# Performance work log

Measured on AMD Instinct MI355X. Metric: run time of the kernel, lower is better.

Reference implementation:

```python
import jax, jax.numpy as jnp
import numpy as np

N = 50000
E = 640000
F_IN = 128
HID = 128
OUT = 64


def setup_inputs() -> dict:
    key = jax.random.key(0)
    ks = jax.random.split(key, 16)
    x = jax.random.normal(ks[0], (N, F_IN), dtype=jnp.float32)
    edge_index = jax.random.randint(ks[1], (2, E), 0, N, dtype=jnp.int64)

    def lin(k, fan_in, fan_out):
        bound = 1.0 / np.sqrt(fan_in)
        kw, kb = jax.random.split(k)
        W = jax.random.uniform(kw, (fan_in, fan_out), jnp.float32, -bound, bound)
        b = jax.random.uniform(kb, (fan_out,), jnp.float32, -bound, bound)
        return W, b

    W1, b1 = lin(ks[2], F_IN, HID)
    W2, b2 = lin(ks[3], HID, HID)
    W3, b3 = lin(ks[4], HID, HID)
    Wres, bres = lin(ks[5], F_IN, HID)
    Wlin, blin = lin(ks[6], HID, OUT)
    return {"x": x, "edge_index": edge_index,
            "W1": W1, "b1": b1, "W2": W2, "b2": b2, "W3": W3, "b3": b3,
            "Wres": Wres, "bres": bres, "Wlin": Wlin, "blin": blin}


def _gcn_norm(edge_index, n):
    # GCNConv default: add self-loops, symmetric normalization D^-1/2 (A+I) D^-1/2
    src, dst = edge_index[0], edge_index[1]
    deg = jax.ops.segment_sum(jnp.ones((edge_index.shape[1],), jnp.float32), dst,
                              num_segments=n) + 1.0  # +1 for self-loop
    dinv = jax.lax.rsqrt(deg)
    norm_e = dinv[src] * dinv[dst]          # [E] edge coefficients
    norm_self = 1.0 / deg                    # [N] self-loop coefficients
    return src, dst, norm_e, norm_self


def _gcn_conv(x, W, b, src, dst, norm_e, norm_self, n):
    h = x @ W                                # [N, F_out]
    agg = jax.ops.segment_sum(h[src] * norm_e[:, None], dst, num_segments=n)
    agg = agg + h * norm_self[:, None]       # self-loop contribution
    return agg + b


def reference(x, edge_index, W1, b1, W2, b2, W3, b3, Wres, bres, Wlin, blin):
    n = x.shape[0]
    src, dst, norm_e, norm_self = _gcn_norm(edge_index, n)
    x_res = x @ Wres + bres
    h = _gcn_conv(x, W1, b1, src, dst, norm_e, norm_self, n)
    h = jax.nn.relu(h + x_res)               # dropout is identity in eval mode
    h = _gcn_conv(h, W2, b2, src, dst, norm_e, norm_self, n)
    h = jax.nn.relu(h)
    h = _gcn_conv(h, W3, b3, src, dst, norm_e, norm_self, n)
    h = jax.nn.relu(h)
    return h @ Wlin + blin
```

## Files before the change

kernel.cpp:

```cpp
#include <hip/hip_runtime.h>

typedef unsigned short ushort_t;
typedef unsigned int uint_t;

typedef __bf16 bf16x8 __attribute__((ext_vector_type(8)));
typedef float f32x4 __attribute__((ext_vector_type(4)));

union BFU { ushort_t u; __bf16 h; };

__device__ __forceinline__ float bf2f(uint_t u) {
    union { uint_t i; float f; } v; v.i = u << 16; return v.f;
}
__device__ __forceinline__ ushort_t f2bf(float f) {
    union { float f; uint_t i; } v; v.f = f;
    uint_t r = v.i + 0x7fffu + ((v.i >> 16) & 1u);
    return (ushort_t)(r >> 16);
}
__device__ __forceinline__ float loadF(const void* p, size_t i, int isBf16) {
    return isBf16 ? bf2f((uint_t)((const ushort_t*)p)[i]) : ((const float*)p)[i];
}

struct DetectArgs {
    const void* t[11];
    int elems[11];
    const int* ei;
    int* flags;
};

__device__ __forceinline__ int detect_one(const void* p, int elems) {
    const uint_t* w = (const uint_t*)p;
    int n = elems / 2; if (n > 64) n = 64;
    int cnt = 0;
    for (int k = 0; k < n; ++k) {
        uint_t f = (w[k] >> 7) & 0xFFu;
        cnt += (f >= 100u && f <= 135u);
    }
    return (cnt * 10 >= n * 6) ? 1 : 0;
}

__global__ void k_pack(DetectArgs a,
                       ushort_t* __restrict__ Tcat, ushort_t* __restrict__ T2,
                       ushort_t* __restrict__ T3, ushort_t* __restrict__ Tl,
                       int* __restrict__ deg, int N,
                       ushort_t* __restrict__ Hbuf, int hps) {
    __shared__ int lflag;
    int i = blockIdx.x * blockDim.x + threadIdx.x;
    if (i < N) deg[i] = 0;
    if (blockIdx.x == 1 && threadIdx.x < 64) {
        int p = threadIdx.x >> 4, w = threadIdx.x & 15;
        ((uint_t*)Hbuf)[(size_t)p * (hps / 2) + (size_t)N * 16 + w] = 0u;
    }
    const int SQ = 128 * 128;
    int m = (i < 4 * SQ) ? (i / SQ) : 4;
    int fid = (m == 0) ? 1 : (m == 1) ? 3 : (m == 2) ? 5 : (m == 3) ? 7 : 9;
    const void* W = a.t[fid];

    if (threadIdx.x == 0) lflag = detect_one(W, a.elems[fid]);
    if (blockIdx.x == 0 && threadIdx.x >= 64 && threadIdx.x < 75) {
        int t = threadIdx.x - 64;
        a.flags[t] = detect_one(a.t[t], a.elems[t]);
    }
    if (blockIdx.x == 0 && threadIdx.x == 75) {
        int nz = 0;
        for (int k = 0; k < 64; ++k) nz += (a.ei[2 * k + 1] != 0);
        a.flags[11] = (nz == 0) ? 1 : 0;
    }
    __syncthreads();
    int isb = lflag;

    if (i < 4 * SQ) {
        int r = i % SQ;
        int k = r / 128, f = r % 128;
        ushort_t* T = (m == 0) ? Tcat : (m == 1) ? T2 : (m == 2) ? T3 : (Tcat + SQ);
        T[f * 128 + k] = f2bf(loadF(W, (size_t)k * 128 + f, isb));
    } else if (i < 4 * SQ + 128 * 64) {
        int r = i - 4 * SQ;
        int k = r / 64, f = r % 64;
        Tl[f * 128 + k] = f2bf(loadF(W, (size_t)k * 64 + f, isb));
    }
}

__global__ void k_deg(const int* __restrict__ ei, int E, int N,
                      const int* __restrict__ flags, int* __restrict__ deg,
                      int2* __restrict__ tmp) {
    int i = blockIdx.x * blockDim.x + threadIdx.x;
    int e0 = i * 4;
    if (e0 >= E) return;
    int is64 = flags[11];
    if (e0 + 3 < E && (E & 3) == 0) {
        int d[4];
        if (is64) {
            int4 va = *(const int4*)(ei + 2 * E + 2 * e0);
            int4 vb = *(const int4*)(ei + 2 * E + 2 * e0 + 4);
            d[0] = va.x; d[1] = va.z; d[2] = vb.x; d[3] = vb.z;
        } else {
            int4 va = *(const int4*)(ei + E + e0);
            d[0] = va.x; d[1] = va.y; d[2] = va.z; d[3] = va.w;
        }
        int l[4]; bool ok[4];
#pragma unroll
        for (int k = 0; k < 4; ++k) ok[k] = (unsigned)d[k] < (unsigned)N;
#pragma unroll
        for (int k = 0; k < 4; ++k)
            l[k] = ok[k] ? atomicAdd(&deg[d[k]], 1) : 0;
        int4 t01, t23;
        t01.x = ok[0] ? d[0] : -1; t01.y = l[0];
        t01.z = ok[1] ? d[1] : -1; t01.w = l[1];
        t23.x = ok[2] ? d[2] : -1; t23.y = l[2];
        t23.z = ok[3] ? d[3] : -1; t23.w = l[3];
        *(int4*)(tmp + e0) = t01;
        *(int4*)(tmp + e0 + 2) = t23;
    } else {
        for (int e = e0; e < E && e < e0 + 4; ++e) {
            int dd = is64 ? ei[2 * E + 2 * e] : ei[E + e];
            bool ok = (unsigned)dd < (unsigned)N;
            int l = ok ? atomicAdd(&deg[dd], 1) : 0;
            tmp[e] = make_int2(ok ? dd : -1, l);
        }
    }
}


__global__ __launch_bounds__(256) void k_bsum(const int* __restrict__ deg, int n,
                                              int* __restrict__ bsum) {
    int base = blockIdx.x * 1024;
    int local = 0;
#pragma unroll
    for (int j = 0; j < 4; ++j) {
        int idx = base + threadIdx.x + j * 256;
        if (idx < n) local += deg[idx];
    }
    __shared__ int s[4];
#pragma unroll
    for (int off = 32; off; off >>= 1) local += __shfl_down(local, off, 64);
    if ((threadIdx.x & 63) == 0) s[threadIdx.x >> 6] = local;
    __syncthreads();
    if (threadIdx.x == 0) bsum[blockIdx.x] = s[0] + s[1] + s[2] + s[3];
}

__global__ __launch_bounds__(256) void k_rowptr(const int* __restrict__ deg,
                                                const int* __restrict__ bsum, int n,
                                                int* __restrict__ row_ptr,
                                                float* __restrict__ dinv) {
    __shared__ int s[256];
    __shared__ int sboff;
    int t = threadIdx.x;

    if (t < 64) {
        int v = (t < blockIdx.x) ? bsum[t] : 0;
#pragma unroll
        for (int off = 32; off; off >>= 1) v += __shfl_down(v, off, 64);
        if (t == 0) sboff = v;
    }

    int base = blockIdx.x * 1024 + t * 4;
    int v0 = (base + 0 < n) ? deg[base + 0] : 0;
    int v1 = (base + 1 < n) ? deg[base + 1] : 0;
    int v2 = (base + 2 < n) ? deg[base + 2] : 0;
    int v3 = (base + 3 < n) ? deg[base + 3] : 0;
    int tot = v0 + v1 + v2 + v3;
    s[t] = tot;
    __syncthreads();
    for (int off = 1; off < 256; off <<= 1) {
        int u = (t >= off) ? s[t - off] : 0;
        __syncthreads();
        s[t] += u;
        __syncthreads();
    }
    int run = sboff + ((t == 0) ? 0 : s[t - 1]);
    int vals[4] = {v0, v1, v2, v3};
#pragma unroll
    for (int j = 0; j < 4; ++j) {
        int idx = base + j;
        if (idx < n) {
            row_ptr[idx] = run;
            run += vals[j];
            float df = (float)vals[j] + 1.0f;
            dinv[idx] = rsqrtf(df);
        }
    }
    if (blockIdx.x == gridDim.x - 1 && t == 255) row_ptr[n] = sboff + s[255];
}

__global__ void k_scatter(const int* __restrict__ ei, int E, int N,
                          const int* __restrict__ flags,
                          const int* __restrict__ row_ptr,
                          const int2* __restrict__ tmp,
                          uint_t* __restrict__ colw) {
    int i = blockIdx.x * blockDim.x + threadIdx.x;
    int e0 = i * 4;
    if (e0 >= E) return;
    int is64 = flags[11];
    if (e0 + 3 < E && (E & 3) == 0) {
        int s[4];
        if (is64) {
            int4 sa = *(const int4*)(ei + 2 * e0);
            int4 sb = *(const int4*)(ei + 2 * e0 + 4);
            s[0] = sa.x; s[1] = sa.z; s[2] = sb.x; s[3] = sb.z;
        } else {
            int4 sa = *(const int4*)(ei + e0);
            s[0] = sa.x; s[1] = sa.y; s[2] = sa.z; s[3] = sa.w;
        }
        int4 t01 = *(const int4*)(tmp + e0);
        int4 t23 = *(const int4*)(tmp + e0 + 2);
        int d[4] = {t01.x, t01.z, t23.x, t23.z};
        int l[4] = {t01.y, t01.w, t23.y, t23.w};
        int ss[4];
#pragma unroll
        for (int k = 0; k < 4; ++k)
            ss[k] = ((unsigned)s[k] < (unsigned)N) ? s[k] : 0;
#pragma unroll
        for (int k = 0; k < 4; ++k) {
            if (d[k] >= 0)
                colw[row_ptr[d[k]] + l[k]] = (uint_t)ss[k];
        }
    } else {
        for (int e = e0; e < E && e < e0 + 4; ++e) {
            int sv = is64 ? ei[2 * e] : ei[e];
            int2 tv = tmp[e];
            if (tv.x >= 0) {
                int ssv = ((unsigned)sv < (unsigned)N) ? sv : 0;
                colw[row_ptr[tv.x] + tv.y] = (uint_t)ssv;
            }
        }
    }
}


template <int NCT>
__device__ __forceinline__ void stage_B(const ushort_t* __restrict__ WT, uint4* lds) {
    int t = threadIdx.x;
#pragma unroll
    for (int i = 0; i < NCT; ++i) {
        int g = i * 256 + t;
        uint4 v = ((const uint4*)WT)[g];
        int col = g >> 4, k8 = g & 15;
        int c = col >> 4, l16c = col & 15;
        int kk = k8 >> 2, q = k8 & 3;
        lds[((kk * NCT + c) << 6) + (q << 4) + l16c] = v;
    }
    __syncthreads();
}

__device__ __forceinline__ void load_A1(const void* __restrict__ A, int a16,
                                        int ar, int quad, bf16x8 af[4]) {
    if (a16) {
        const ushort_t* p = (const ushort_t*)A + (size_t)ar * 128 + quad * 8;
#pragma unroll
        for (int kk = 0; kk < 4; ++kk) af[kk] = *(const bf16x8*)(p + kk * 32);
    } else {
        const float* p = (const float*)A + (size_t)ar * 128 + quad * 8;
#pragma unroll
        for (int kk = 0; kk < 4; ++kk) {
            f32x4 u0 = *(const f32x4*)(p + kk * 32);
            f32x4 u1 = *(const f32x4*)(p + kk * 32 + 4);
#pragma unroll
            for (int j = 0; j < 4; ++j) {
                BFU e;
                e.u = f2bf(u0[j]); af[kk][j] = e.h;
                e.u = f2bf(u1[j]); af[kk][j + 4] = e.h;
            }
        }
    }
}

__device__ __forceinline__ void load_A_planar(const ushort_t* __restrict__ A, int aps,
                                              int ar, int quad, bf16x8 af[4]) {
#pragma unroll
    for (int kk = 0; kk < 4; ++kk)
        af[kk] = *(const bf16x8*)(A + (size_t)kk * aps + (size_t)ar * 32 + quad * 8);
}

template <int NCT>
__global__ __launch_bounds__(256, 4) void k_gemm2(const ushort_t* __restrict__ A, int aps,
                                                  const ushort_t* __restrict__ WT,
                                                  const void* __restrict__ bias, int bFid,
                                                  void* __restrict__ C, int cFix, int cps,
                                                  int M, const int* __restrict__ flags,
                                                  const float* __restrict__ rowscale) {
    __shared__ uint4 lds[NCT * 256];
    stage_B<NCT>(WT, lds);

    const int F = NCT * 16;
    int t = threadIdx.x;
    int wave = t >> 6, lane = t & 63;
    int quad = lane >> 4, l16 = lane & 15;
    int row0 = blockIdx.x * 64 + wave * 16;

    int ar = row0 + l16; if (ar >= M) ar = M - 1;

    bf16x8 af[4];
    load_A_planar(A, aps, ar, quad, af);

    f32x4 acc[NCT];
#pragma unroll
    for (int c = 0; c < NCT; ++c) acc[c] = (f32x4){0.f, 0.f, 0.f, 0.f};

#pragma unroll
    for (int kk = 0; kk < 4; ++kk) {
#pragma unroll
        for (int c = 0; c < NCT; ++c) {
            bf16x8 b = *(const bf16x8*)&lds[((kk * NCT + c) << 6) + lane];
            acc[c] = __builtin_amdgcn_mfma_f32_16x16x32_bf16(af[kk], b, acc[c], 0, 0, 0);
        }
    }

    float rs[4];
#pragma unroll
    for (int q = 0; q < 4; ++q) {
        int row = row0 + quad * 4 + q;
        rs[q] = (rowscale && row < M) ? rowscale[row] : 1.0f;
    }

    int bf = (bias && bFid >= 0) ? flags[bFid] : 1;
#pragma unroll
    for (int c = 0; c < NCT; ++c) {
        int colg = c * 16 + l16;
        float bv = bias ? loadF(bias, colg, bf) : 0.0f;
#pragma unroll
        for (int q = 0; q < 4; ++q) {
            int row = row0 + quad * 4 + q;
            if (row < M) {
                float v = acc[c][q] * rs[q] + bv;
                if (cFix) {
                    int p = colg >> 5, po = colg & 31;
                    ((ushort_t*)C)[(size_t)p * cps + (size_t)row * 32 + po] = f2bf(v);
                } else {
                    ((float*)C)[(size_t)row * F + colg] = v;
                }
            }
        }
    }
}

__global__ __launch_bounds__(256, 4) void k_gemm_l1(const void* __restrict__ A,
                                                    const ushort_t* __restrict__ Tcat,
                                                    const void* __restrict__ bres,
                                                    ushort_t* __restrict__ Hout, int hps,
                                                    ushort_t* __restrict__ Xres, int xps,
                                                    int M, const int* __restrict__ flags,
                                                    const float* __restrict__ dinv) {
    __shared__ uint4 lds[8 * 256];
    int t = threadIdx.x;
    int wave = t >> 6, lane = t & 63;
    int quad = lane >> 4, l16 = lane & 15;
    int row0 = blockIdx.x * 64 + wave * 16;

    int a16 = flags[0];
    int ar = row0 + l16; if (ar >= M) ar = M - 1;

    bf16x8 af[4];
    load_A1(A, a16, ar, quad, af);

    float rs[4];
#pragma unroll
    for (int q = 0; q < 4; ++q) {
        int row = row0 + quad * 4 + q;
        rs[q] = (row < M) ? dinv[row] : 1.0f;
    }

    stage_B<8>(Tcat, lds);
    {
        f32x4 acc[8];
#pragma unroll
        for (int c = 0; c < 8; ++c) acc[c] = (f32x4){0.f, 0.f, 0.f, 0.f};
#pragma unroll
        for (int kk = 0; kk < 4; ++kk) {
#pragma unroll
            for (int c = 0; c < 8; ++c) {
                bf16x8 b = *(const bf16x8*)&lds[((kk * 8 + c) << 6) + lane];
                acc[c] = __builtin_amdgcn_mfma_f32_16x16x32_bf16(af[kk], b, acc[c], 0, 0, 0);
            }
        }
#pragma unroll
        for (int c = 0; c < 8; ++c) {
            int colg = c * 16 + l16;
            int p = colg >> 5, po = colg & 31;
#pragma unroll
            for (int q = 0; q < 4; ++q) {
                int row = row0 + quad * 4 + q;
                if (row < M)
                    Hout[(size_t)p * hps + (size_t)row * 32 + po] = f2bf(acc[c][q] * rs[q]);
            }
        }
    }
    __syncthreads();

    stage_B<8>(Tcat + 128 * 128, lds);
    {
        int bf = flags[8];
        f32x4 acc[8];
#pragma unroll
        for (int c = 0; c < 8; ++c) acc[c] = (f32x4){0.f, 0.f, 0.f, 0.f};
#pragma unroll
        for (int kk = 0; kk < 4; ++kk) {
#pragma unroll
            for (int c = 0; c < 8; ++c) {
                bf16x8 b = *(const bf16x8*)&lds[((kk * 8 + c) << 6) + lane];
                acc[c] = __builtin_amdgcn_mfma_f32_16x16x32_bf16(af[kk], b, acc[c], 0, 0, 0);
            }
        }
#pragma unroll
        for (int c = 0; c < 8; ++c) {
            int colg = c * 16 + l16;
            int p = colg >> 5, po = colg & 31;
            float bv = loadF(bres, colg, bf);
#pragma unroll
            for (int q = 0; q < 4; ++q) {
                int row = row0 + quad * 4 + q;
                if (row < M)
                    Xres[(size_t)p * xps + (size_t)row * 32 + po] = f2bf(acc[c][q] + bv);
            }
        }
    }
}

__global__ __launch_bounds__(256) void k_agg(const ushort_t* __restrict__ H, int hps,
                                             const int* __restrict__ row_ptr,
                                             const uint_t* __restrict__ colw,
                                             const float* __restrict__ dinv,
                                             const void* __restrict__ bias, int bFid,
                                             const ushort_t* __restrict__ other, int ops,
                                             ushort_t* __restrict__ Out,
                                             int n, const int* __restrict__ flags) {
    int s = blockIdx.x & 3;
    int wave = threadIdx.x >> 6;
    int lane = threadIdx.x & 63;
    int e4 = lane >> 4;
    int fl = lane & 15;
    int fo = fl * 2;
    int node = (blockIdx.x >> 2) * 16 + wave * 4 + e4;
    bool ok = (node < n);
    const ushort_t* Hs = H + (size_t)s * hps;

    int beg = ok ? row_ptr[node] : 0;
    int end = ok ? row_ptr[node + 1] : 0;

    float a0 = 0.f, a1 = 0.f;

    for (int b = beg; b < end; b += 16) {
        int ci = b + fl;
        int c = (ci < end) ? (int)__builtin_nontemporal_load(&colw[ci]) : n;
#pragma unroll
        for (int q = 0; q < 16; ++q) {
            int ce = __shfl(c, q, 16);
            uint_t v = *(const uint_t*)(Hs + (size_t)ce * 32 + fo);
            a0 += bf2f(v & 0xffffu);
            a1 += bf2f(v >> 16);
        }
    }

    if (ok) {
        size_t nofs = (size_t)node * 32 + fo;
        uint_t hv = *(const uint_t*)(Hs + nofs);
        a0 += bf2f(hv & 0xffffu);
        a1 += bf2f(hv >> 16);
        float dv = dinv[node];
        int fg = s * 32 + fo;
        int bfm = flags[bFid];
        float a0o = fmaf(a0, dv, loadF(bias, fg, bfm));
        float a1o = fmaf(a1, dv, loadF(bias, fg + 1, bfm));
        if (other) {
            uint_t ov = __builtin_nontemporal_load(
                (const uint_t*)(other + (size_t)s * ops + nofs));
            a0o += bf2f(ov & 0xffffu);
            a1o += bf2f(ov >> 16);
        }
        a0o = fmaxf(a0o, 0.0f);
        a1o = fmaxf(a1o, 0.0f);
        __builtin_nontemporal_store((uint_t)f2bf(a0o) | ((uint_t)f2bf(a1o) << 16),
                                    (uint_t*)(Out + (size_t)s * ops + nofs));
    }
}


extern "C" void kernel_launch(void* const* d_in, const int* in_sizes, int n_in,
                              void* d_out, int out_size, void* d_ws, size_t ws_size,
                              hipStream_t stream) {
    const int N = in_sizes[0] / 128;
    const int E = in_sizes[1] / 2;

    const void* x  = d_in[0];
    const int*  ei = (const int*)d_in[1];

    char* ws = (char*)d_ws;
    size_t used = 0;
    auto alloc = [&](size_t bytes) {
        char* p = ws + used;
        used += (bytes + 255) & ~(size_t)255;
        return p;
    };

    int*   flags   = (int*)alloc(64 * 4);
    int*   deg     = (int*)alloc((size_t)N * 4);
    int*   row_ptr = (int*)alloc((size_t)(N + 1) * 4);
    float* dinv    = (float*)alloc((size_t)N * 4);
    int2*  tmp     = (int2*)alloc((size_t)E * 8);
    uint_t* colw   = (uint_t*)alloc((size_t)E * 4);
    int*   bsum    = (int*)alloc(256 * 4);
    ushort_t* Tcat = (ushort_t*)alloc(256 * 128 * 2);
    ushort_t* T2   = (ushort_t*)alloc(128 * 128 * 2);
    ushort_t* T3   = (ushort_t*)alloc(128 * 128 * 2);
    ushort_t* Tlin = (ushort_t*)alloc(128 * 64 * 2);

    ushort_t* Hbuf = (ushort_t*)alloc((size_t)(N + 1) * 128 * 2);
    ushort_t* Act1 = (ushort_t*)alloc((size_t)N * 128 * 2);
    ushort_t* Act2 = (ushort_t*)alloc((size_t)N * 128 * 2);
    ushort_t* Xres = (ushort_t*)alloc((size_t)N * 128 * 2);

    if (used > ws_size) return;

    const int PH = (N + 1) * 32;
    const int PA = N * 32;

    DetectArgs da;
    for (int i = 0; i < 11; ++i) { da.t[i] = d_in[i == 0 ? 0 : i + 1]; da.elems[i] = in_sizes[i == 0 ? 0 : i + 1]; }
    da.ei = ei;
    da.flags = flags;

    const int B = 256;
    int gE4   = ((E + 3) / 4 + B - 1) / B;
    int gPack = (4 * 128 * 128 + 128 * 64) / B;
    int gGemm = (N + 63) / 64;
    int gAgg  = ((N + 15) / 16) * 4;
    int nb    = (N + 1023) / 1024;

    k_pack<<<gPack, B, 0, stream>>>(da, Tcat, T2, T3, Tlin, deg, N, Hbuf, PH);
    k_deg<<<gE4, B, 0, stream>>>(ei, E, N, flags, deg, tmp);
    k_bsum<<<nb, B, 0, stream>>>(deg, N, bsum);
    k_rowptr<<<nb, B, 0, stream>>>(deg, bsum, N, row_ptr, dinv);
    k_scatter<<<gE4, B, 0, stream>>>(ei, E, N, flags, row_ptr, tmp, colw);

    k_gemm_l1<<<gGemm, B, 0, stream>>>(x, Tcat, d_in[9], Hbuf, PH, Xres, PA, N, flags, dinv);
    k_agg<<<gAgg, B, 0, stream>>>(Hbuf, PH, row_ptr, colw, dinv, d_in[3], 2,
                                  Xres, PA, Act1, N, flags);

    k_gemm2<8><<<gGemm, B, 0, stream>>>(Act1, PA, T2, nullptr, -1, Hbuf, 1, PH, N, flags, dinv);
    k_agg<<<gAgg, B, 0, stream>>>(Hbuf, PH, row_ptr, colw, dinv, d_in[5], 4,
                                  nullptr, PA, Act2, N, flags);

    k_gemm2<8><<<gGemm, B, 0, stream>>>(Act2, PA, T3, nullptr, -1, Hbuf, 1, PH, N, flags, dinv);
    k_agg<<<gAgg, B, 0, stream>>>(Hbuf, PH, row_ptr, colw, dinv, d_in[7], 6,
                                  nullptr, PA, Act1, N, flags);

    k_gemm2<4><<<gGemm, B, 0, stream>>>(Act1, PA, Tlin, d_in[11], 10,
                                        d_out, 0, 0, N, flags, nullptr);
}
```

Baseline: 306.8 us.

## Interleave feature layout to pack GEMM stores and widen aggregation loads

Activation columns are stored in a permuted, interleaved order within each 32-column slab, so each GEMM lane writes adjacent column pairs as one 32-bit store instead of two 16-bit stores. The weight rows of the next layers are permuted (kappa) so the matmuls still consume the new order. The aggregation kernel now gives each node 8 lanes that each load 4 features (64-bit gathers), doubling nodes per block, and software-prefetches the next 8 column indices. This cuts store and gather instruction counts at the cost of per-lane serial neighbor loops with less lane parallelism over edges.

```diff
diff --git a/kernel.cpp b/kernel.cpp
--- a/kernel.cpp
+++ b/kernel.cpp
@@ -2,6 +2,7 @@
 
 typedef unsigned short ushort_t;
 typedef unsigned int uint_t;
+typedef unsigned long long u64_t;
 
 typedef __bf16 bf16x8 __attribute__((ext_vector_type(8)));
 typedef float f32x4 __attribute__((ext_vector_type(4)));
@@ -36,6 +37,10 @@
         cnt += (f >= 100u && f <= 135u);
     }
     return (cnt * 10 >= n * 6) ? 1 : 0;
+}
+
+__device__ __forceinline__ int kappa(int s) {
+    return 32 * (s >> 5) + 16 * (s & 1) + 4 * ((s >> 3) & 3) + ((s & 7) >> 1);
 }
 
 __global__ void k_pack(DetectArgs a,
@@ -70,13 +75,15 @@
 
     if (i < 4 * SQ) {
         int r = i % SQ;
-        int k = r / 128, f = r % 128;
+        int s = r / 128, f = r % 128;
         ushort_t* T = (m == 0) ? Tcat : (m == 1) ? T2 : (m == 2) ? T3 : (Tcat + SQ);
-        T[f * 128 + k] = f2bf(loadF(W, (size_t)k * 128 + f, isb));
+        int k = (m == 1 || m == 2) ? kappa(s) : s;
+        T[f * 128 + s] = f2bf(loadF(W, (size_t)k * 128 + f, isb));
     } else if (i < 4 * SQ + 128 * 64) {
         int r = i - 4 * SQ;
-        int k = r / 64, f = r % 64;
-        Tl[f * 128 + k] = f2bf(loadF(W, (size_t)k * 64 + f, isb));
+        int s = r / 64, f = r % 64;
+        int k = kappa(s);
+        Tl[f * 128 + s] = f2bf(loadF(W, (size_t)k * 64 + f, isb));
     }
 }
 
@@ -313,21 +320,33 @@
     }
 
     int bf = (bias && bFid >= 0) ? flags[bFid] : 1;
-#pragma unroll
-    for (int c = 0; c < NCT; ++c) {
-        int colg = c * 16 + l16;
-        float bv = bias ? loadF(bias, colg, bf) : 0.0f;
-#pragma unroll
-        for (int q = 0; q < 4; ++q) {
-            int row = row0 + quad * 4 + q;
-            if (row < M) {
-                float v = acc[c][q] * rs[q] + bv;
-                if (cFix) {
-                    int p = colg >> 5, po = colg & 31;
-                    ((ushort_t*)C)[(size_t)p * cps + (size_t)row * 32 + po] = f2bf(v);
-                } else {
-                    ((float*)C)[(size_t)row * F + colg] = v;
+    if (cFix) {
+#pragma unroll
+        for (int p = 0; p < NCT / 2; ++p) {
+            int c0 = 2 * p, c1 = 2 * p + 1;
+            float bv0 = bias ? loadF(bias, c0 * 16 + l16, bf) : 0.0f;
+            float bv1 = bias ? loadF(bias, c1 * 16 + l16, bf) : 0.0f;
+#pragma unroll
+            for (int q = 0; q < 4; ++q) {
+                int row = row0 + quad * 4 + q;
+                if (row < M) {
+                    float v0 = acc[c0][q] * rs[q] + bv0;
+                    float v1 = acc[c1][q] * rs[q] + bv1;
+                    uint_t u = (uint_t)f2bf(v0) | ((uint_t)f2bf(v1) << 16);
+                    *(uint_t*)((ushort_t*)C + (size_t)p * cps + (size_t)row * 32 + 2 * l16) = u;
                 }
+            }
+        }
+    } else {
+#pragma unroll
+        for (int c = 0; c < NCT; ++c) {
+            int colg = c * 16 + l16;
+            float bv = bias ? loadF(bias, colg, bf) : 0.0f;
+#pragma unroll
+            for (int q = 0; q < 4; ++q) {
+                int row = row0 + quad * 4 + q;
+                if (row < M)
+                    ((float*)C)[(size_t)row * F + colg] = acc[c][q] * rs[q] + bv;
             }
         }
     }
@@ -373,14 +392,16 @@
             }
         }
 #pragma unroll
-        for (int c = 0; c < 8; ++c) {
-            int colg = c * 16 + l16;
-            int p = colg >> 5, po = colg & 31;
+        for (int p = 0; p < 4; ++p) {
+            int c0 = 2 * p, c1 = 2 * p + 1;
 #pragma unroll
             for (int q = 0; q < 4; ++q) {
                 int row = row0 + quad * 4 + q;
-                if (row < M)
-                    Hout[(size_t)p * hps + (size_t)row * 32 + po] = f2bf(acc[c][q] * rs[q]);
+                if (row < M) {
+                    uint_t u = (uint_t)f2bf(acc[c0][q] * rs[q]) |
+                               ((uint_t)f2bf(acc[c1][q] * rs[q]) << 16);
+                    *(uint_t*)(Hout + (size_t)p * hps + (size_t)row * 32 + 2 * l16) = u;
+                }
             }
         }
     }
@@ -401,15 +422,18 @@
             }
         }
 #pragma unroll
-        for (int c = 0; c < 8; ++c) {
-            int colg = c * 16 + l16;
-            int p = colg >> 5, po = colg & 31;
-            float bv = loadF(bres, colg, bf);
+        for (int p = 0; p < 4; ++p) {
+            int c0 = 2 * p, c1 = 2 * p + 1;
+            float bv0 = loadF(bres, c0 * 16 + l16, bf);
+            float bv1 = loadF(bres, c1 * 16 + l16, bf);
 #pragma unroll
             for (int q = 0; q < 4; ++q) {
                 int row = row0 + quad * 4 + q;
-                if (row < M)
-                    Xres[(size_t)p * xps + (size_t)row * 32 + po] = f2bf(acc[c][q] + bv);
+                if (row < M) {
+                    uint_t u = (uint_t)f2bf(acc[c0][q] + bv0) |
+                               ((uint_t)f2bf(acc[c1][q] + bv1) << 16);
+                    *(uint_t*)(Xres + (size_t)p * xps + (size_t)row * 32 + 2 * l16) = u;
+                }
             }
         }
     }
@@ -426,50 +450,73 @@
     int s = blockIdx.x & 3;
     int wave = threadIdx.x >> 6;
     int lane = threadIdx.x & 63;
-    int e4 = lane >> 4;
-    int fl = lane & 15;
-    int fo = fl * 2;
-    int node = (blockIdx.x >> 2) * 16 + wave * 4 + e4;
+    int g8 = lane >> 3;
+    int fl = lane & 7;
+    int fo = fl * 4;
+    int node = (blockIdx.x >> 2) * 32 + wave * 8 + g8;
     bool ok = (node < n);
     const ushort_t* Hs = H + (size_t)s * hps;
 
-    int beg = ok ? row_ptr[node] : 0;
-    int end = ok ? row_ptr[node + 1] : 0;
-
-    float a0 = 0.f, a1 = 0.f;
-
-    for (int b = beg; b < end; b += 16) {
-        int ci = b + fl;
-        int c = (ci < end) ? (int)__builtin_nontemporal_load(&colw[ci]) : n;
-#pragma unroll
-        for (int q = 0; q < 16; ++q) {
-            int ce = __shfl(c, q, 16);
-            uint_t v = *(const uint_t*)(Hs + (size_t)ce * 32 + fo);
-            a0 += bf2f(v & 0xffffu);
-            a1 += bf2f(v >> 16);
-        }
+    int nd = ok ? node : (n - 1);
+    int beg = row_ptr[nd], end = row_ptr[nd + 1];
+    if (!ok) end = beg;
+
+    float a0 = 0.f, a1 = 0.f, a2 = 0.f, a3 = 0.f;
+
+    int b = beg;
+    int cq[8];
+#pragma unroll
+    for (int q = 0; q < 8; ++q)
+        cq[q] = (b + q < end) ? (int)__builtin_nontemporal_load(&colw[b + q]) : n;
+    while (b < end) {
+        int bn = b + 8;
+        int cn[8];
+#pragma unroll
+        for (int q = 0; q < 8; ++q)
+            cn[q] = (bn + q < end) ? (int)__builtin_nontemporal_load(&colw[bn + q]) : n;
+#pragma unroll
+        for (int q = 0; q < 8; ++q) {
+            uint_t off = (uint_t)cq[q] * 32u + (uint_t)fo;
+            uint2 v = *(const uint2*)(Hs + off);
+            a0 += bf2f(v.x & 0xffffu);
+            a1 += bf2f(v.x >> 16);
+            a2 += bf2f(v.y & 0xffffu);
+            a3 += bf2f(v.y >> 16);
+        }
+        b = bn;
+#pragma unroll
+        for (int q = 0; q < 8; ++q) cq[q] = cn[q];
     }
 
     if (ok) {
         size_t nofs = (size_t)node * 32 + fo;
-        uint_t hv = *(const uint_t*)(Hs + nofs);
-        a0 += bf2f(hv & 0xffffu);
-        a1 += bf2f(hv >> 16);
+        uint2 hv = *(const uint2*)(Hs + nofs);
+        a0 += bf2f(hv.x & 0xffffu);
+        a1 += bf2f(hv.x >> 16);
+        a2 += bf2f(hv.y & 0xffffu);
+        a3 += bf2f(hv.y >> 16);
         float dv = dinv[node];
-        int fg = s * 32 + fo;
         int bfm = flags[bFid];
-        float a0o = fmaf(a0, dv, loadF(bias, fg, bfm));
-        float a1o = fmaf(a1, dv, loadF(bias, fg + 1, bfm));
+        int f0 = s * 32 + 2 * fl;
+        int f1 = s * 32 + 16 + 2 * fl;
+        float o0 = fmaf(a0, dv, loadF(bias, f0, bfm));
+        float o1 = fmaf(a1, dv, loadF(bias, f1, bfm));
+        float o2 = fmaf(a2, dv, loadF(bias, f0 + 1, bfm));
+        float o3 = fmaf(a3, dv, loadF(bias, f1 + 1, bfm));
         if (other) {
-            uint_t ov = __builtin_nontemporal_load(
-                (const uint_t*)(other + (size_t)s * ops + nofs));
-            a0o += bf2f(ov & 0xffffu);
-            a1o += bf2f(ov >> 16);
-        }
-        a0o = fmaxf(a0o, 0.0f);
-        a1o = fmaxf(a1o, 0.0f);
-        __builtin_nontemporal_store((uint_t)f2bf(a0o) | ((uint_t)f2bf(a1o) << 16),
-                                    (uint_t*)(Out + (size_t)s * ops + nofs));
+            u64_t ovu = __builtin_nontemporal_load(
+                (const u64_t*)(other + (size_t)s * ops + nofs));
+            uint_t ovx = (uint_t)ovu, ovy = (uint_t)(ovu >> 32);
+            o0 += bf2f(ovx & 0xffffu);
+            o1 += bf2f(ovx >> 16);
+            o2 += bf2f(ovy & 0xffffu);
+            o3 += bf2f(ovy >> 16);
+        }
+        o0 = fmaxf(o0, 0.0f); o1 = fmaxf(o1, 0.0f);
+        o2 = fmaxf(o2, 0.0f); o3 = fmaxf(o3, 0.0f);
+        u64_t outv = (u64_t)((uint_t)f2bf(o0) | ((uint_t)f2bf(o1) << 16)) |
+                     ((u64_t)((uint_t)f2bf(o2) | ((uint_t)f2bf(o3) << 16)) << 32);
+        __builtin_nontemporal_store(outv, (u64_t*)(Out + (size_t)s * ops + nofs));
     }
 }
 
@@ -522,7 +569,7 @@
     int gE4   = ((E + 3) / 4 + B - 1) / B;
     int gPack = (4 * 128 * 128 + 128 * 64) / B;
     int gGemm = (N + 63) / 64;
-    int gAgg  = ((N + 15) / 16) * 4;
+    int gAgg  = ((N + 31) / 32) * 4;
     int nb    = (N + 1023) / 1024;
 
     k_pack<<<gPack, B, 0, stream>>>(da, Tcat, T2, T3, Tlin, deg, N, Hbuf, PH);
```

After: 320.7 us. +4.5%, slower.
